# Kernel optimization log

Hardware: AMD Instinct MI355X
Metric: run time of the kernel (lower is better)

## Reference

```python
import jax, jax.numpy as jnp
import numpy as np

N, E, P, D, G, L = 100000, 640000, 640000, 128, 128, 3
BN_EPS = 1e-5

def _bn(x, p):
    # eval-mode BatchNorm1d: p is stacked [gamma, beta, running_mean, running_var]
    g, b, m, v = p[0], p[1], p[2], p[3]
    return (x - m) * jax.lax.rsqrt(v + BN_EPS) * g + b

def setup_inputs() -> dict:
    key = jax.random.key(0)
    ks = iter(jax.random.split(key, 64))
    def nrm(shape, s):
        return jax.random.normal(next(ks), shape, jnp.float32) * s
    def bnp(shape):
        return jax.random.uniform(next(ks), shape, jnp.float32, 0.5, 1.5)
    inp = {}
    # graph data
    inp['x_node'] = jnp.zeros((N,), jnp.int32)
    inp['edge_index'] = jax.random.randint(next(ks), (2, E), 0, N, jnp.int32)
    inp['edge_attr'] = jax.random.normal(next(ks), (E, 7), jnp.float32)
    inp['batch'] = jnp.sort(jax.random.randint(next(ks), (N,), 0, G, jnp.int32))
    inp['pos_index'] = jax.random.randint(next(ks), (P,), 0, 1800, jnp.int32)
    inp['pos_enc'] = jax.random.uniform(next(ks), (P,), jnp.float32)
    inp['pos_batch'] = jnp.sort(jax.random.randint(next(ks), (P,), 0, E, jnp.int32))
    # encoders
    inp['node_emb'] = nrm((1, D), 1.0)                 # Embedding(1, D) for ogbg-ppa
    inp['z_init'] = nrm((1800, D), 1.0)                # z_initial embedding table
    inp['ze_bn1'] = bnp((4, D))
    inp['ze_W'] = nrm((D, D), D ** -0.5)
    inp['ze_b'] = jnp.zeros((D,), jnp.float32)
    inp['ze_bn2'] = bnp((4, D))
    inp['vn_emb'] = jnp.zeros((1, D), jnp.float32)     # init.constant_(0)
    # GINConv_eff per-layer params (stacked over L)
    inp['conv_We'] = nrm((L, 7, D), 7 ** -0.5)         # edge_encoder Linear(7, D)
    inp['conv_be'] = jnp.zeros((L, D), jnp.float32)
    inp['conv_Wp'] = nrm((L, D, D), D ** -0.5)         # edge_encoder_pos Linear(D, D)
    inp['conv_bp'] = jnp.zeros((L, D), jnp.float32)
    inp['conv_W1'] = nrm((L, D, 2 * D), D ** -0.5)     # mlp Linear(D, 2D)
    inp['conv_b1'] = jnp.zeros((L, 2 * D), jnp.float32)
    inp['conv_bn'] = bnp((L, 4, 2 * D))                # mlp BatchNorm(2D)
    inp['conv_W2'] = nrm((L, 2 * D, D), (2 * D) ** -0.5)  # mlp Linear(2D, D)
    inp['conv_b2'] = jnp.zeros((L, D), jnp.float32)
    inp['conv_eps'] = jnp.zeros((L,), jnp.float32)     # GIN eps, init 0
    inp['layer_bn'] = bnp((L, 4, D))                   # per-layer batch_norms
    # virtual-node MLPs (L-1 of them)
    inp['vn_W1'] = nrm((L - 1, D, 2 * D), D ** -0.5)
    inp['vn_b1'] = jnp.zeros((L - 1, 2 * D), jnp.float32)
    inp['vn_bn1'] = bnp((L - 1, 4, 2 * D))
    inp['vn_W2'] = nrm((L - 1, 2 * D, D), (2 * D) ** -0.5)
    inp['vn_b2'] = jnp.zeros((L - 1, D), jnp.float32)
    inp['vn_bn2'] = bnp((L - 1, 4, D))
    return inp

def reference(x_node, edge_index, edge_attr, batch, pos_index, pos_enc, pos_batch,
              node_emb, z_init, ze_bn1, ze_W, ze_b, ze_bn2, vn_emb,
              conv_We, conv_be, conv_Wp, conv_bp, conv_W1, conv_b1, conv_bn,
              conv_W2, conv_b2, conv_eps, layer_bn,
              vn_W1, vn_b1, vn_bn1, vn_W2, vn_b2, vn_bn2):
    src, dst = edge_index[0], edge_index[1]
    # node encoder (Embedding(1, D) indexed by zeros)
    h = node_emb[x_node]                                           # [N, D]
    # positional edge embedding: pool z_initial rows per edge, then z_embedding MLP
    z = jax.ops.segment_sum(z_init[pos_index] * pos_enc[:, None], pos_batch,
                            num_segments=E)                        # [E, D]
    z = jax.nn.relu(_bn(z, ze_bn1))
    z = jax.nn.relu(_bn(z @ ze_W + ze_b, ze_bn2))
    # virtual node embeddings, one per graph
    vn = jnp.broadcast_to(vn_emb[0], (G, D))
    for l in range(L):
        h_in = h + vn[batch]                                       # virtual-node broadcast add
        # GINConv_eff
        edge_emb = edge_attr @ conv_We[l] + conv_be[l] + z @ conv_Wp[l] + conv_bp[l]  # [E, D]
        msg = jax.nn.relu(h_in[src] + edge_emb)                    # gather + relu
        agg = jax.ops.segment_sum(msg, dst, num_segments=N)        # scatter-add
        t = (1.0 + conv_eps[l]) * h_in + agg
        t = jax.nn.relu(_bn(t @ conv_W1[l] + conv_b1[l], conv_bn[l]))
        out = t @ conv_W2[l] + conv_b2[l]
        out = _bn(out, layer_bn[l])                                # batch_norms[l]
        h = out if l == L - 1 else jax.nn.relu(out)                # dropout is identity (eval)
        if l < L - 1:
            vt = jax.ops.segment_sum(h_in, batch, num_segments=G) + vn
            vt = jax.nn.relu(_bn(vt @ vn_W1[l] + vn_b1[l], vn_bn1[l]))
            vn = jax.nn.relu(_bn(vt @ vn_W2[l] + vn_b2[l], vn_bn2[l]))
    return h  # JK == 'last'
```

## Files before the change

kernel.cpp:

```cpp
#include <hip/hip_runtime.h>
#include <hip/hip_bf16.h>

typedef __hip_bfloat16 bf16;
typedef __attribute__((ext_vector_type(8))) short short8;
typedef __attribute__((ext_vector_type(4))) float floatx4;

constexpr int Nn = 100000;
constexpr int Ee = 640000;
constexpr int Pp = 640000;
constexpr int Gg = 128;
constexpr int Ll = 3;
#define Dd 128
#define BN_EPS 1e-5f

__device__ __forceinline__ float b2f(bf16 x) { return __bfloat162float(x); }
__device__ __forceinline__ bf16 f2b(float x) { return __float2bfloat16(x); }

union U8 { uint4 u; bf16 h[8]; short8 s; };

__global__ void k_estart(const int* __restrict__ pos_batch, int* __restrict__ estart) {
  int e = blockIdx.x * blockDim.x + threadIdx.x;
  if (e > Ee) return;
  int lo = 0, hi = Pp;
  while (lo < hi) { int mid = (lo + hi) >> 1; if (pos_batch[mid] < e) lo = mid + 1; else hi = mid; }
  estart[e] = lo;
}

__global__ void k_hist(const int* __restrict__ dst, int* __restrict__ cnt) {
  int e = blockIdx.x * blockDim.x + threadIdx.x;
  if (e >= Ee) return;
  atomicAdd(&cnt[dst[e]], 1);
}

__global__ void k_scanA(const int* __restrict__ cnt, int* __restrict__ rs,
                        int* __restrict__ chunkSum) {
  __shared__ int buf[1024];
  int tid = threadIdx.x;
  int i = blockIdx.x * 1024 + tid;
  int v = (i < Nn) ? cnt[i] : 0;
  buf[tid] = v;
  __syncthreads();
  for (int off = 1; off < 1024; off <<= 1) {
    int t = (tid >= off) ? buf[tid - off] : 0;
    __syncthreads();
    buf[tid] += t;
    __syncthreads();
  }
  if (i < Nn) rs[i] = buf[tid] - v;
  if (tid == 1023) chunkSum[blockIdx.x] = buf[1023];
}

__global__ void k_scanC(int* __restrict__ rs, const int* __restrict__ chunkSum) {
  __shared__ int offS;
  if (threadIdx.x == 0) {
    int o = 0;
    for (int j = 0; j < blockIdx.x; ++j) o += chunkSum[j];
    offS = o;
  }
  __syncthreads();
  int i = blockIdx.x * 1024 + threadIdx.x;
  if (i < Nn) rs[i] += offS;
}

__global__ void k_scatter(const int* __restrict__ dst, const int* __restrict__ rs,
                          int* __restrict__ cur, int* __restrict__ perm) {
  int e = blockIdx.x * blockDim.x + threadIdx.x;
  if (e >= Ee) return;
  int d = dst[e];
  int r = atomicAdd(&cur[d], 1);
  perm[rs[d] + r] = e;
}

__global__ void k_permcopy(const int* __restrict__ perm, const int* __restrict__ src,
                           const int* __restrict__ dst, const int* __restrict__ estart,
                           const float* __restrict__ eattr,
                           int* __restrict__ src_p, int* __restrict__ dst_p,
                           int2* __restrict__ rng_p, bf16* __restrict__ ea_p) {
  int i = blockIdx.x * blockDim.x + threadIdx.x;
  if (i >= Ee) return;
  int e = perm[i];
  src_p[i] = src[e];
  dst_p[i] = dst[e];
  rng_p[i] = make_int2(estart[e], estart[e + 1]);
  U8 o;
  #pragma unroll
  for (int j = 0; j < 7; ++j) o.h[j] = f2b(eattr[(size_t)e * 7 + j]);
  o.h[7] = f2b(1.0f);
  ((uint4*)ea_p)[i] = o.u;
}

__global__ void k_prep(const float* __restrict__ zeW, const float* __restrict__ Wp,
                       const float* __restrict__ We, const float* __restrict__ be,
                       const float* __restrict__ bp,
                       const float* __restrict__ W1, const float* __restrict__ W2,
                       bf16* __restrict__ zeWsw, bf16* __restrict__ WpSw,
                       bf16* __restrict__ WeSw, bf16* __restrict__ W1sw,
                       bf16* __restrict__ W2sw) {
  int gid = blockIdx.x * blockDim.x + threadIdx.x;
  if (gid < 16384) {
    int i = gid;
    int j = i & 7, lane = (i >> 3) & 63, t = (i >> 9) & 7, kc = i >> 12;
    int k = kc * 32 + ((lane >> 4) * 8) + j, n = t * 16 + (lane & 15);
    zeWsw[i] = f2b(zeW[k * 128 + n]);
  }
  if (gid < 49152) {
    int l = gid / 16384, i = gid % 16384;
    int j = i & 7, lane = (i >> 3) & 63, t = (i >> 9) & 7, kc = i >> 12;
    int k = kc * 32 + ((lane >> 4) * 8) + j, n = t * 16 + (lane & 15);
    WpSw[gid] = f2b(Wp[l * 16384 + k * 128 + n]);
  }
  if (gid < 12288) {
    int l = gid / 4096, i = gid % 4096;
    int j = i & 7, lane = (i >> 3) & 63, t = i >> 9;
    int k = ((lane >> 4) * 8) + j, n = t * 16 + (lane & 15);
    float v = 0.f;
    if (k < 7) v = We[l * 896 + k * 128 + n];
    else if (k == 7) v = be[l * 128 + n] + bp[l * 128 + n];
    WeSw[gid] = f2b(v);
  }
  if (gid < 98304) {
    int l = gid / 32768, i = gid % 32768;
    int j = i & 7, lane = (i >> 3) & 63, t = (i >> 9) & 15, kc = i >> 13;
    int k = kc * 32 + ((lane >> 4) * 8) + j, n = t * 16 + (lane & 15);
    W1sw[gid] = f2b(W1[l * 32768 + k * 256 + n]);
  }
  if (gid < 98304) {
    int l = gid / 32768, i = gid % 32768;
    int j = i & 7, lane = (i >> 3) & 63, t = (i >> 9) & 7, kc = i >> 12;
    int k = kc * 32 + ((lane >> 4) * 8) + j, n = t * 16 + (lane & 15);
    W2sw[gid] = f2b(W2[l * 32768 + k * 128 + n]);
  }
}

__global__ void k_bnfold(const float* __restrict__ ze_bn1, const float* __restrict__ ze_b,
                         const float* __restrict__ ze_bn2,
                         const float* __restrict__ conv_b1, const float* __restrict__ conv_bn,
                         const float* __restrict__ conv_b2, const float* __restrict__ layer_bn,
                         const float* __restrict__ vn_b1, const float* __restrict__ vn_bn1,
                         const float* __restrict__ vn_b2, const float* __restrict__ vn_bn2,
                         float* __restrict__ fb) {
  int i = blockIdx.x * blockDim.x + threadIdx.x;
  if (i < 128) {
    float g = ze_bn1[i], b = ze_bn1[128 + i], m = ze_bn1[256 + i], v = ze_bn1[384 + i];
    float s = g * rsqrtf(v + BN_EPS);
    fb[i] = s; fb[128 + i] = b - m * s;
  } else if (i < 256) {
    int c = i - 128;
    float g = ze_bn2[c], b = ze_bn2[128 + c], m = ze_bn2[256 + c], v = ze_bn2[384 + c];
    float s = g * rsqrtf(v + BN_EPS);
    fb[256 + c] = s; fb[384 + c] = b - m * s + s * ze_b[c];
  } else if (i < 1024) {
    int j = i - 256; int l = j >> 8, c = j & 255;
    const float* bn = conv_bn + (size_t)l * 1024;
    float g = bn[c], b = bn[256 + c], m = bn[512 + c], v = bn[768 + c];
    float s = g * rsqrtf(v + BN_EPS);
    fb[512 + j] = s; fb[1280 + j] = b - m * s + s * conv_b1[l * 256 + c];
  } else if (i < 1408) {
    int j = i - 1024; int l = j >> 7, c = j & 127;
    const float* bn = layer_bn + (size_t)l * 512;
    float g = bn[c], b = bn[128 + c], m = bn[256 + c], v = bn[384 + c];
    float s = g * rsqrtf(v + BN_EPS);
    fb[2048 + j] = s; fb[2432 + j] = b - m * s + s * conv_b2[l * 128 + c];
  } else if (i < 1920) {
    int j = i - 1408; int l = j >> 8, c = j & 255;
    const float* bn = vn_bn1 + (size_t)l * 1024;
    float g = bn[c], b = bn[256 + c], m = bn[512 + c], v = bn[768 + c];
    float s = g * rsqrtf(v + BN_EPS);
    fb[2816 + j] = s; fb[3328 + j] = b - m * s + s * vn_b1[l * 256 + c];
  } else if (i < 2176) {
    int j = i - 1920; int l = j >> 7, c = j & 127;
    const float* bn = vn_bn2 + (size_t)l * 512;
    float g = bn[c], b = bn[128 + c], m = bn[256 + c], v = bn[384 + c];
    float s = g * rsqrtf(v + BN_EPS);
    fb[3840 + j] = s; fb[4096 + j] = b - m * s + s * vn_b2[l * 128 + c];
  }
}

__global__ void k_init_vn(const float* __restrict__ vn_emb, float* __restrict__ vn) {
  int gid = blockIdx.x * blockDim.x + threadIdx.x;
  if (gid >= Gg * 128) return;
  vn[gid] = vn_emb[gid & 127];
}

__global__ void k_hin0(const int* __restrict__ x_node, const float* __restrict__ node_emb,
                       const float* __restrict__ vn, const int* __restrict__ batch,
                       bf16* __restrict__ h_in) {
  int gid = blockIdx.x * blockDim.x + threadIdx.x;
  if (gid >= Nn * 16) return;
  int n = gid >> 4, c = gid & 15;
  int x = x_node[n], b = batch[n];
  float4 a0 = ((const float4*)node_emb)[x * 32 + c * 2];
  float4 a1 = ((const float4*)node_emb)[x * 32 + c * 2 + 1];
  float4 v0 = ((const float4*)vn)[b * 32 + c * 2];
  float4 v1 = ((const float4*)vn)[b * 32 + c * 2 + 1];
  U8 o;
  o.h[0] = f2b(a0.x + v0.x); o.h[1] = f2b(a0.y + v0.y);
  o.h[2] = f2b(a0.z + v0.z); o.h[3] = f2b(a0.w + v0.w);
  o.h[4] = f2b(a1.x + v1.x); o.h[5] = f2b(a1.y + v1.y);
  o.h[6] = f2b(a1.z + v1.z); o.h[7] = f2b(a1.w + v1.w);
  ((uint4*)h_in)[gid] = o.u;
}

__global__ void k_hin(const float* __restrict__ vn, const int* __restrict__ batch,
                      bf16* __restrict__ h_in) {
  int gid = blockIdx.x * blockDim.x + threadIdx.x;
  if (gid >= Nn * 16) return;
  int n = gid >> 4, c = gid & 15;
  U8 a; a.u = ((const uint4*)h_in)[gid];
  int b = batch[n];
  float4 v0 = ((const float4*)vn)[b * 32 + c * 2];
  float4 v1 = ((const float4*)vn)[b * 32 + c * 2 + 1];
  U8 o;
  o.h[0] = f2b(b2f(a.h[0]) + v0.x); o.h[1] = f2b(b2f(a.h[1]) + v0.y);
  o.h[2] = f2b(b2f(a.h[2]) + v0.z); o.h[3] = f2b(b2f(a.h[3]) + v0.w);
  o.h[4] = f2b(b2f(a.h[4]) + v1.x); o.h[5] = f2b(b2f(a.h[5]) + v1.y);
  o.h[6] = f2b(b2f(a.h[6]) + v1.z); o.h[7] = f2b(b2f(a.h[7]) + v1.w);
  ((uint4*)h_in)[gid] = o.u;
}

__global__ __launch_bounds__(256, 4) void k_zemb(
    const int2* __restrict__ rng_perm, const int* __restrict__ pos_index,
    const float* __restrict__ pos_enc, const float* __restrict__ z_init,
    const float* __restrict__ fb, const bf16* __restrict__ zeWsw,
    bf16* __restrict__ Z) {
  __shared__ bf16 Az[64][136];
  int tid = threadIdx.x;
  int lane = tid & 63, wv = tid >> 6;
  int q = lane >> 4, ln = lane & 15;
  int e0 = blockIdx.x * 64;

  {
    int r = lane >> 2, cc = lane & 3;
    int2 rg = rng_perm[e0 + 16 * wv + r];
    float acc[32];
    #pragma unroll
    for (int j = 0; j < 32; ++j) acc[j] = 0.f;
    for (int p = rg.x; p < rg.y; ++p) {
      int idx = pos_index[p];
      float w = pos_enc[p];
      #pragma unroll
      for (int qq = 0; qq < 8; ++qq) {
        float4 z4 = ((const float4*)z_init)[idx * 32 + cc * 8 + qq];
        acc[qq * 4 + 0] = fmaf(w, z4.x, acc[qq * 4 + 0]);
        acc[qq * 4 + 1] = fmaf(w, z4.y, acc[qq * 4 + 1]);
        acc[qq * 4 + 2] = fmaf(w, z4.z, acc[qq * 4 + 2]);
        acc[qq * 4 + 3] = fmaf(w, z4.w, acc[qq * 4 + 3]);
      }
    }
    #pragma unroll
    for (int qq = 0; qq < 4; ++qq) {
      U8 o;
      #pragma unroll
      for (int jj = 0; jj < 2; ++jj) {
        int col = cc * 32 + qq * 8 + jj * 4;
        float4 s4 = *(const float4*)&fb[col];
        float4 h4 = *(const float4*)&fb[128 + col];
        o.h[jj * 4 + 0] = f2b(fmaxf(0.f, fmaf(acc[qq * 8 + jj * 4 + 0], s4.x, h4.x)));
        o.h[jj * 4 + 1] = f2b(fmaxf(0.f, fmaf(acc[qq * 8 + jj * 4 + 1], s4.y, h4.y)));
        o.h[jj * 4 + 2] = f2b(fmaxf(0.f, fmaf(acc[qq * 8 + jj * 4 + 2], s4.z, h4.z)));
        o.h[jj * 4 + 3] = f2b(fmaxf(0.f, fmaf(acc[qq * 8 + jj * 4 + 3], s4.w, h4.w)));
      }
      *(uint4*)&Az[16 * wv + r][cc * 32 + qq * 8] = o.u;
    }
  }
  __builtin_amdgcn_wave_barrier();

  floatx4 acc1[8] = {};
  #pragma unroll
  for (int kc = 0; kc < 4; ++kc) {
    short8 af = *(const short8*)&Az[16 * wv + ln][kc * 32 + q * 8];
    #pragma unroll
    for (int t = 0; t < 8; ++t) {
      short8 bfr = *(const short8*)(zeWsw + (((size_t)kc * 8 + t) * 64 + lane) * 8);
      acc1[t] = __builtin_amdgcn_mfma_f32_16x16x32_bf16(af, bfr, acc1[t], 0, 0, 0);
    }
  }
  #pragma unroll
  for (int t = 0; t < 8; ++t) {
    int c = t * 16 + ln;
    float ss = fb[256 + c], hh = fb[384 + c];
    #pragma unroll
    for (int r = 0; r < 4; ++r)
      Az[16 * wv + q * 4 + r][c] = f2b(fmaxf(0.f, fmaf(acc1[t][r], ss, hh)));
  }
  __builtin_amdgcn_wave_barrier();
  #pragma unroll
  for (int p = 0; p < 4; ++p) {
    int row = 16 * wv + p * 4 + q;
    uint4 vv = *(const uint4*)&Az[row][ln * 8];
    ((uint4*)Z)[(size_t)(e0 + row) * 16 + ln] = vv;
  }
}

__global__ __launch_bounds__(256, 6) void k_edge_fused(
    const bf16* __restrict__ Z, const bf16* __restrict__ ea_p,
    const int* __restrict__ src_p, const int* __restrict__ dst_p,
    const bf16* __restrict__ h_in,
    const bf16* __restrict__ WpSw, const bf16* __restrict__ WeSw,
    float* agg) {
  __shared__ bf16 Az[64][136];
  __shared__ int dstS[64];
  int tid = threadIdx.x;
  int lane = tid & 63, wv = tid >> 6;
  int q = lane >> 4, ln = lane & 15;
  int e0 = blockIdx.x * 64;

  if (q == 0) dstS[16 * wv + ln] = dst_p[e0 + 16 * wv + ln];

  short8 af0 = {};
  if (q == 0) af0 = *(const short8*)(ea_p + (size_t)(e0 + 16 * wv + ln) * 8);
  const bf16* zrow = Z + (size_t)(e0 + 16 * wv + ln) * 128 + q * 8;
  short8 zf0 = *(const short8*)(zrow);
  short8 zf1 = *(const short8*)(zrow + 32);
  short8 zf2 = *(const short8*)(zrow + 64);
  short8 zf3 = *(const short8*)(zrow + 96);

  #pragma unroll
  for (int p = 0; p < 4; ++p) {
    int el = 16 * wv + p * 4 + q;
    int s = src_p[e0 + el];
    uint4 hh = ((const uint4*)h_in)[(size_t)s * 16 + ln];
    *(uint4*)&Az[el][ln * 8] = hh;
  }

  floatx4 acc2[8] = {};
  #pragma unroll
  for (int t = 0; t < 8; ++t) {
    short8 bfr = *(const short8*)(WeSw + ((size_t)t * 64 + lane) * 8);
    acc2[t] = __builtin_amdgcn_mfma_f32_16x16x32_bf16(af0, bfr, acc2[t], 0, 0, 0);
  }
  #pragma unroll
  for (int t = 0; t < 8; ++t) {
    short8 bfr = *(const short8*)(WpSw + ((size_t)t * 64 + lane) * 8);
    acc2[t] = __builtin_amdgcn_mfma_f32_16x16x32_bf16(zf0, bfr, acc2[t], 0, 0, 0);
  }
  #pragma unroll
  for (int t = 0; t < 8; ++t) {
    short8 bfr = *(const short8*)(WpSw + (((size_t)8 + t) * 64 + lane) * 8);
    acc2[t] = __builtin_amdgcn_mfma_f32_16x16x32_bf16(zf1, bfr, acc2[t], 0, 0, 0);
  }
  #pragma unroll
  for (int t = 0; t < 8; ++t) {
    short8 bfr = *(const short8*)(WpSw + (((size_t)16 + t) * 64 + lane) * 8);
    acc2[t] = __builtin_amdgcn_mfma_f32_16x16x32_bf16(zf2, bfr, acc2[t], 0, 0, 0);
  }
  #pragma unroll
  for (int t = 0; t < 8; ++t) {
    short8 bfr = *(const short8*)(WpSw + (((size_t)24 + t) * 64 + lane) * 8);
    acc2[t] = __builtin_amdgcn_mfma_f32_16x16x32_bf16(zf3, bfr, acc2[t], 0, 0, 0);
  }
  __builtin_amdgcn_wave_barrier();
  #pragma unroll
  for (int t = 0; t < 8; ++t) {
    int c = t * 16 + ln;
    #pragma unroll
    for (int r = 0; r < 4; ++r) {
      int el = 16 * wv + q * 4 + r;
      Az[el][c] = f2b(fmaxf(0.f, acc2[t][r] + b2f(Az[el][c])));
    }
  }
  __builtin_amdgcn_wave_barrier();
  {
    float s0 = 0.f, s1 = 0.f;
    int dprev = dstS[16 * wv];
    bool inside = false;
    #pragma unroll
    for (int j = 0; j < 16; ++j) {
      int dcur = dstS[16 * wv + j];
      if (dcur != dprev) {
        float* ap = agg + (size_t)dprev * Dd;
        if (inside) { ap[lane] = s0; ap[64 + lane] = s1; }
        else        { atomicAdd(ap + lane, s0); atomicAdd(ap + 64 + lane, s1); }
        s0 = 0.f; s1 = 0.f; dprev = dcur; inside = true;
      }
      s0 += b2f(Az[16 * wv + j][lane]);
      s1 += b2f(Az[16 * wv + j][64 + lane]);
    }
    float* ap = agg + (size_t)dprev * Dd;
    atomicAdd(ap + lane, s0);
    atomicAdd(ap + 64 + lane, s1);
  }
}

__global__ __launch_bounds__(256, 4) void k_edge_full(
    const int2* __restrict__ rng_perm, const int* __restrict__ pos_index,
    const float* __restrict__ pos_enc, const float* __restrict__ z_init,
    const float* __restrict__ fb, const bf16* __restrict__ zeWsw,
    const bf16* __restrict__ ea_p, const int* __restrict__ src_p,
    const int* __restrict__ dst_p, const bf16* __restrict__ h_in,
    const bf16* __restrict__ WpSw, const bf16* __restrict__ WeSw,
    float* agg) {
  __shared__ bf16 Az[64][136];
  __shared__ int dstS[64];
  int tid = threadIdx.x;
  int lane = tid & 63, wv = tid >> 6;
  int q = lane >> 4, ln = lane & 15;
  int e0 = blockIdx.x * 64;

  if (q == 0) dstS[16 * wv + ln] = dst_p[e0 + 16 * wv + ln];
  short8 af0 = {};
  if (q == 0) af0 = *(const short8*)(ea_p + (size_t)(e0 + 16 * wv + ln) * 8);

  {
    int r = lane >> 2, cc = lane & 3;
    int2 rg = rng_perm[e0 + 16 * wv + r];
    float acc[32];
    #pragma unroll
    for (int j = 0; j < 32; ++j) acc[j] = 0.f;
    for (int p = rg.x; p < rg.y; ++p) {
      int idx = pos_index[p];
      float w = pos_enc[p];
      #pragma unroll
      for (int qq = 0; qq < 8; ++qq) {
        float4 z4 = ((const float4*)z_init)[idx * 32 + cc * 8 + qq];
        acc[qq * 4 + 0] = fmaf(w, z4.x, acc[qq * 4 + 0]);
        acc[qq * 4 + 1] = fmaf(w, z4.y, acc[qq * 4 + 1]);
        acc[qq * 4 + 2] = fmaf(w, z4.z, acc[qq * 4 + 2]);
        acc[qq * 4 + 3] = fmaf(w, z4.w, acc[qq * 4 + 3]);
      }
    }
    #pragma unroll
    for (int qq = 0; qq < 4; ++qq) {
      U8 o;
      #pragma unroll
      for (int jj = 0; jj < 2; ++jj) {
        int col = cc * 32 + qq * 8 + jj * 4;
        float4 s4 = *(const float4*)&fb[col];
        float4 h4 = *(const float4*)&fb[128 + col];
        o.h[jj * 4 + 0] = f2b(fmaxf(0.f, fmaf(acc[qq * 8 + jj * 4 + 0], s4.x, h4.x)));
        o.h[jj * 4 + 1] = f2b(fmaxf(0.f, fmaf(acc[qq * 8 + jj * 4 + 1], s4.y, h4.y)));
        o.h[jj * 4 + 2] = f2b(fmaxf(0.f, fmaf(acc[qq * 8 + jj * 4 + 2], s4.z, h4.z)));
        o.h[jj * 4 + 3] = f2b(fmaxf(0.f, fmaf(acc[qq * 8 + jj * 4 + 3], s4.w, h4.w)));
      }
      *(uint4*)&Az[16 * wv + r][cc * 32 + qq * 8] = o.u;
    }
  }
  __builtin_amdgcn_wave_barrier();

  floatx4 acc2[8] = {};
  #pragma unroll
  for (int t = 0; t < 8; ++t) {
    short8 bfr = *(const short8*)(WeSw + ((size_t)t * 64 + lane) * 8);
    acc2[t] = __builtin_amdgcn_mfma_f32_16x16x32_bf16(af0, bfr, acc2[t], 0, 0, 0);
  }
  floatx4 acc1[8] = {};
  #pragma unroll
  for (int kc = 0; kc < 4; ++kc) {
    short8 af = *(const short8*)&Az[16 * wv + ln][kc * 32 + q * 8];
    #pragma unroll
    for (int t = 0; t < 8; ++t) {
      short8 bfr = *(const short8*)(zeWsw + (((size_t)kc * 8 + t) * 64 + lane) * 8);
      acc1[t] = __builtin_amdgcn_mfma_f32_16x16x32_bf16(af, bfr, acc1[t], 0, 0, 0);
    }
  }
  #pragma unroll
  for (int t = 0; t < 8; ++t) {
    int c = t * 16 + ln;
    float ss = fb[256 + c], hh = fb[384 + c];
    #pragma unroll
    for (int r = 0; r < 4; ++r)
      Az[16 * wv + q * 4 + r][c] = f2b(fmaxf(0.f, fmaf(acc1[t][r], ss, hh)));
  }
  __builtin_amdgcn_wave_barrier();
  #pragma unroll
  for (int kc = 0; kc < 4; ++kc) {
    short8 af = *(const short8*)&Az[16 * wv + ln][kc * 32 + q * 8];
    #pragma unroll
    for (int t = 0; t < 8; ++t) {
      short8 bfr = *(const short8*)(WpSw + (((size_t)kc * 8 + t) * 64 + lane) * 8);
      acc2[t] = __builtin_amdgcn_mfma_f32_16x16x32_bf16(af, bfr, acc2[t], 0, 0, 0);
    }
  }
  __builtin_amdgcn_wave_barrier();
  #pragma unroll
  for (int p = 0; p < 4; ++p) {
    int el = 16 * wv + p * 4 + q;
    int s = src_p[e0 + el];
    uint4 hh = ((const uint4*)h_in)[(size_t)s * 16 + ln];
    *(uint4*)&Az[el][ln * 8] = hh;
  }
  __builtin_amdgcn_wave_barrier();
  #pragma unroll
  for (int t = 0; t < 8; ++t) {
    int c = t * 16 + ln;
    #pragma unroll
    for (int r = 0; r < 4; ++r) {
      int el = 16 * wv + q * 4 + r;
      Az[el][c] = f2b(fmaxf(0.f, acc2[t][r] + b2f(Az[el][c])));
    }
  }
  __builtin_amdgcn_wave_barrier();
  {
    float s0 = 0.f, s1 = 0.f;
    int dprev = dstS[16 * wv];
    bool inside = false;
    #pragma unroll
    for (int j = 0; j < 16; ++j) {
      int dcur = dstS[16 * wv + j];
      if (dcur != dprev) {
        float* ap = agg + (size_t)dprev * Dd;
        if (inside) { ap[lane] = s0; ap[64 + lane] = s1; }
        else        { atomicAdd(ap + lane, s0); atomicAdd(ap + 64 + lane, s1); }
        s0 = 0.f; s1 = 0.f; dprev = dcur; inside = true;
      }
      s0 += b2f(Az[16 * wv + j][lane]);
      s1 += b2f(Az[16 * wv + j][64 + lane]);
    }
    float* ap = agg + (size_t)dprev * Dd;
    atomicAdd(ap + lane, s0);
    atomicAdd(ap + 64 + lane, s1);
  }
}

__global__ __launch_bounds__(256) void k_mlp_fused(
    const bf16* __restrict__ h_in, const float* agg,
    const float* __restrict__ eps_arr, int l,
    const bf16* __restrict__ W1sw, const float* __restrict__ Msc, const float* __restrict__ Msh,
    const bf16* __restrict__ W2sw, const float* __restrict__ Lsc, const float* __restrict__ Lsh,
    int is_last, bf16* __restrict__ out_b, float* out_f) {
  __shared__ bf16 R[4][16][280];
  int tid = threadIdx.x;
  int lane = tid & 63, wv = tid >> 6;
  int q = lane >> 4, ln = lane & 15;
  int r0 = blockIdx.x * 64;
  float epsv = 1.0f + eps_arr[l];
  {
    int r = lane >> 2, cc = lane & 3;
    int row = r0 + 16 * wv + r;
    #pragma unroll
    for (int u = 0; u < 4; ++u) {
      int cb = cc * 4 + u;
      U8 o;
      if (row < Nn) {
        U8 hh; hh.u = ((const uint4*)h_in)[row * 16 + cb];
        float4 g0 = ((const float4*)agg)[row * 32 + cb * 2];
        float4 g1 = ((const float4*)agg)[row * 32 + cb * 2 + 1];
        o.h[0] = f2b(epsv * b2f(hh.h[0]) + g0.x); o.h[1] = f2b(epsv * b2f(hh.h[1]) + g0.y);
        o.h[2] = f2b(epsv * b2f(hh.h[2]) + g0.z); o.h[3] = f2b(epsv * b2f(hh.h[3]) + g0.w);
        o.h[4] = f2b(epsv * b2f(hh.h[4]) + g1.x); o.h[5] = f2b(epsv * b2f(hh.h[5]) + g1.y);
        o.h[6] = f2b(epsv * b2f(hh.h[6]) + g1.z); o.h[7] = f2b(epsv * b2f(hh.h[7]) + g1.w);
      } else {
        o.u.x = o.u.y = o.u.z = o.u.w = 0;
      }
      *(uint4*)&R[wv][r][cb * 8] = o.u;
    }
  }
  __builtin_amdgcn_wave_barrier();
  floatx4 acc1[16] = {};
  #pragma unroll
  for (int kc = 0; kc < 4; ++kc) {
    short8 af = *(const short8*)&R[wv][ln][kc * 32 + q * 8];
    #pragma unroll
    for (int t = 0; t < 16; ++t) {
      short8 bfr = *(const short8*)(W1sw + (size_t)l * 32768 + (((size_t)kc * 16 + t) * 64 + lane) * 8);
      acc1[t] = __builtin_amdgcn_mfma_f32_16x16x32_bf16(af, bfr, acc1[t], 0, 0, 0);
    }
  }
  #pragma unroll
  for (int t = 0; t < 16; ++t) {
    int c = t * 16 + ln;
    float ss = Msc[c], hh = Msh[c];
    #pragma unroll
    for (int r = 0; r < 4; ++r)
      R[wv][q * 4 + r][c] = f2b(fmaxf(0.f, fmaf(acc1[t][r], ss, hh)));
  }
  __builtin_amdgcn_wave_barrier();
  floatx4 acc2[8] = {};
  #pragma unroll
  for (int kc = 0; kc < 8; ++kc) {
    short8 af = *(const short8*)&R[wv][ln][kc * 32 + q * 8];
    #pragma unroll
    for (int t = 0; t < 8; ++t) {
      short8 bfr = *(const short8*)(W2sw + (size_t)l * 32768 + (((size_t)kc * 8 + t) * 64 + lane) * 8);
      acc2[t] = __builtin_amdgcn_mfma_f32_16x16x32_bf16(af, bfr, acc2[t], 0, 0, 0);
    }
  }
  #pragma unroll
  for (int t = 0; t < 8; ++t) {
    int c = t * 16 + ln;
    float ss = Lsc[c], hh = Lsh[c];
    #pragma unroll
    for (int r = 0; r < 4; ++r) {
      int row = r0 + 16 * wv + q * 4 + r;
      if (row < Nn) {
        float x = fmaf(acc2[t][r], ss, hh);
        if (is_last) out_f[(size_t)row * Dd + c] = x;
        else         out_b[(size_t)row * Dd + c] = f2b(fmaxf(0.f, x));
      }
    }
  }
}

__global__ void k_vt_sum(const bf16* __restrict__ h_in, const int* __restrict__ batch,
                         float* __restrict__ vt) {
  int d = threadIdx.x;
  int chunk = (Nn + gridDim.x - 1) / gridDim.x;
  int r0 = blockIdx.x * chunk;
  int r1 = min(r0 + chunk, Nn);
  if (r0 >= r1) return;
  float acc = 0.f;
  int cur = batch[r0];
  for (int r = r0; r < r1; ++r) {
    int g = batch[r];
    if (g != cur) { atomicAdd(&vt[cur * Dd + d], acc); acc = 0.f; cur = g; }
    acc += b2f(h_in[r * Dd + d]);
  }
  atomicAdd(&vt[cur * Dd + d], acc);
}

__global__ __launch_bounds__(256) void k_vn_mlp(
    float* __restrict__ vn, const float* __restrict__ vt,
    const float* __restrict__ W1, const float* __restrict__ s1, const float* __restrict__ h1,
    const float* __restrict__ W2, const float* __restrict__ s2, const float* __restrict__ h2) {
  __shared__ float row[128];
  __shared__ float trow[256];
  int g = blockIdx.x;
  int tid = threadIdx.x;
  if (tid < 128) row[tid] = vt[g * Dd + tid] + vn[g * Dd + tid];
  __syncthreads();
  float acc = 0.f;
  for (int k = 0; k < 128; ++k) acc += row[k] * W1[k * 256 + tid];
  trow[tid] = fmaxf(0.f, fmaf(acc, s1[tid], h1[tid]));
  __syncthreads();
  if (tid < 128) {
    float acc2 = 0.f;
    for (int k = 0; k < 256; ++k) acc2 += trow[k] * W2[k * Dd + tid];
    vn[g * Dd + tid] = fmaxf(0.f, fmaf(acc2, s2[tid], h2[tid]));
  }
}

extern "C" void kernel_launch(void* const* d_in, const int* in_sizes, int n_in,
                              void* d_out, int out_size, void* d_ws, size_t ws_size,
                              hipStream_t stream) {
  const int*   x_node    = (const int*)  d_in[0];
  const int*   edge_idx  = (const int*)  d_in[1];
  const float* edge_attr = (const float*)d_in[2];
  const int*   batch     = (const int*)  d_in[3];
  const int*   pos_index = (const int*)  d_in[4];
  const float* pos_enc   = (const float*)d_in[5];
  const int*   pos_batch = (const int*)  d_in[6];
  const float* node_emb  = (const float*)d_in[7];
  const float* z_init    = (const float*)d_in[8];
  const float* ze_bn1    = (const float*)d_in[9];
  const float* ze_W      = (const float*)d_in[10];
  const float* ze_b      = (const float*)d_in[11];
  const float* ze_bn2    = (const float*)d_in[12];
  const float* vn_emb    = (const float*)d_in[13];
  const float* conv_We   = (const float*)d_in[14];
  const float* conv_be   = (const float*)d_in[15];
  const float* conv_Wp   = (const float*)d_in[16];
  const float* conv_bp   = (const float*)d_in[17];
  const float* conv_W1   = (const float*)d_in[18];
  const float* conv_b1   = (const float*)d_in[19];
  const float* conv_bn   = (const float*)d_in[20];
  const float* conv_W2   = (const float*)d_in[21];
  const float* conv_b2   = (const float*)d_in[22];
  const float* conv_eps  = (const float*)d_in[23];
  const float* layer_bn  = (const float*)d_in[24];
  const float* vn_W1     = (const float*)d_in[25];
  const float* vn_b1     = (const float*)d_in[26];
  const float* vn_bn1    = (const float*)d_in[27];
  const float* vn_W2     = (const float*)d_in[28];
  const float* vn_b2     = (const float*)d_in[29];
  const float* vn_bn2    = (const float*)d_in[30];

  char* wb = (char*)d_ws;
  size_t o = 0;
  auto alloc = [&](size_t bytes) { void* p = wb + o; o += (bytes + 255) & ~255ull; return p; };
  bf16*  h_in     = (bf16*) alloc((size_t)Nn * 128 * 2);
  float* vn       = (float*)alloc((size_t)Gg * 128 * 4);
  float* vt       = (float*)alloc((size_t)Gg * 128 * 4);
  int*   estart   = (int*)  alloc((size_t)(Ee + 1) * 4);
  bf16*  zeWsw    = (bf16*) alloc(16384 * 2);
  bf16*  WpSw     = (bf16*) alloc(49152 * 2);
  bf16*  WeSw     = (bf16*) alloc(12288 * 2);
  bf16*  W1sw     = (bf16*) alloc(98304 * 2);
  bf16*  W2sw     = (bf16*) alloc(98304 * 2);
  float* fb       = (float*)alloc(4352 * 4);
  int*   cnt      = (int*)  alloc((size_t)Nn * 4);
  int*   rs       = (int*)  alloc((size_t)Nn * 4);
  int*   cur      = (int*)  alloc((size_t)Nn * 4);
  int*   chunkSum = (int*)  alloc(128 * 4);
  int*   perm     = (int*)  alloc((size_t)Ee * 4);
  int*   src_p    = (int*)  alloc((size_t)Ee * 4);
  int*   dst_p    = (int*)  alloc((size_t)Ee * 4);
  int2*  rng_p    = (int2*) alloc((size_t)Ee * 8);
  bf16*  ea_p     = (bf16*) alloc((size_t)Ee * 8 * 2);
  bf16*  Z        = (bf16*) alloc((size_t)Ee * 128 * 2);
  float* agg      = (float*)d_out;
  bool useZ = (o <= ws_size);

  const int* src = edge_idx;
  const int* dst = edge_idx + Ee;

  k_estart<<<(Ee + 256) / 256, 256, 0, stream>>>(pos_batch, estart);
  hipMemsetAsync(cnt, 0, (size_t)Nn * 4, stream);
  hipMemsetAsync(cur, 0, (size_t)Nn * 4, stream);
  k_hist<<<(Ee + 255) / 256, 256, 0, stream>>>(dst, cnt);
  int nchunk = (Nn + 1023) / 1024;
  k_scanA<<<nchunk, 1024, 0, stream>>>(cnt, rs, chunkSum);
  k_scanC<<<nchunk, 1024, 0, stream>>>(rs, chunkSum);
  k_scatter<<<(Ee + 255) / 256, 256, 0, stream>>>(dst, rs, cur, perm);
  k_permcopy<<<(Ee + 255) / 256, 256, 0, stream>>>(perm, src, dst, estart, edge_attr,
                                                   src_p, dst_p, rng_p, ea_p);
  k_prep<<<(98304 + 255) / 256, 256, 0, stream>>>(ze_W, conv_Wp, conv_We, conv_be, conv_bp,
                                                  conv_W1, conv_W2,
                                                  zeWsw, WpSw, WeSw, W1sw, W2sw);
  k_bnfold<<<9, 256, 0, stream>>>(ze_bn1, ze_b, ze_bn2, conv_b1, conv_bn,
                                  conv_b2, layer_bn, vn_b1, vn_bn1, vn_b2, vn_bn2, fb);
  k_init_vn<<<(Gg * 128 + 255) / 256, 256, 0, stream>>>(vn_emb, vn);
  if (useZ)
    k_zemb<<<Ee / 64, 256, 0, stream>>>(rng_p, pos_index, pos_enc, z_init, fb, zeWsw, Z);

  int hblocks = (Nn * 16 + 255) / 256;
  int mblocks = (Nn + 63) / 64;
  for (int l = 0; l < Ll; ++l) {
    if (l == 0) k_hin0<<<hblocks, 256, 0, stream>>>(x_node, node_emb, vn, batch, h_in);
    else        k_hin <<<hblocks, 256, 0, stream>>>(vn, batch, h_in);
    hipMemsetAsync(agg, 0, (size_t)Nn * 128 * 4, stream);
    if (useZ)
      k_edge_fused<<<Ee / 64, 256, 0, stream>>>(Z, ea_p, src_p, dst_p, h_in,
          WpSw + (size_t)l * 16384, WeSw + (size_t)l * 4096, agg);
    else
      k_edge_full<<<Ee / 64, 256, 0, stream>>>(rng_p, pos_index, pos_enc, z_init,
          fb, zeWsw, ea_p, src_p, dst_p, h_in,
          WpSw + (size_t)l * 16384, WeSw + (size_t)l * 4096, agg);
    if (l < Ll - 1) {
      hipMemsetAsync(vt, 0, (size_t)Gg * 128 * 4, stream);
      k_vt_sum<<<1024, 128, 0, stream>>>(h_in, batch, vt);
      k_vn_mlp<<<Gg, 256, 0, stream>>>(vn, vt,
          vn_W1 + (size_t)l * 128 * 256, fb + 2816 + l * 256, fb + 3328 + l * 256,
          vn_W2 + (size_t)l * 256 * 128, fb + 3840 + l * 128, fb + 4096 + l * 128);
    }
    k_mlp_fused<<<mblocks, 256, 0, stream>>>(h_in, agg, conv_eps, l,
        W1sw, fb + 512 + l * 256, fb + 1280 + l * 256,
        W2sw, fb + 2048 + l * 128, fb + 2432 + l * 128,
        (l == Ll - 1) ? 1 : 0, h_in, (float*)d_out);
  }
}
```

Measured before the change: 1.257 ms.

## Fuse z-embedding into first edge layer and fold vn-add and agg zeroing into MLP

The separate z-embedding kernel is merged into the first layer's edge kernel, which now computes Z, optionally stores it for later layers, and performs the message/aggregation step in the same launch. The per-layer h_in virtual-node add kernel is removed: k_mlp_fused adds vn[batch] to its output and zeroes agg rows as it consumes them, replacing the per-layer memset. This cuts several full passes over node and edge arrays and a few launches. In exchange the MLP epilogue carries extra gathers, and correctness depends on vn being updated before k_mlp_fused runs, which the stream order provides.

```diff
diff --git a/kernel.cpp b/kernel.cpp
--- a/kernel.cpp
+++ b/kernel.cpp
@@ -201,33 +201,24 @@
   ((uint4*)h_in)[gid] = o.u;
 }
 
-__global__ void k_hin(const float* __restrict__ vn, const int* __restrict__ batch,
-                      bf16* __restrict__ h_in) {
-  int gid = blockIdx.x * blockDim.x + threadIdx.x;
-  if (gid >= Nn * 16) return;
-  int n = gid >> 4, c = gid & 15;
-  U8 a; a.u = ((const uint4*)h_in)[gid];
-  int b = batch[n];
-  float4 v0 = ((const float4*)vn)[b * 32 + c * 2];
-  float4 v1 = ((const float4*)vn)[b * 32 + c * 2 + 1];
-  U8 o;
-  o.h[0] = f2b(b2f(a.h[0]) + v0.x); o.h[1] = f2b(b2f(a.h[1]) + v0.y);
-  o.h[2] = f2b(b2f(a.h[2]) + v0.z); o.h[3] = f2b(b2f(a.h[3]) + v0.w);
-  o.h[4] = f2b(b2f(a.h[4]) + v1.x); o.h[5] = f2b(b2f(a.h[5]) + v1.y);
-  o.h[6] = f2b(b2f(a.h[6]) + v1.z); o.h[7] = f2b(b2f(a.h[7]) + v1.w);
-  ((uint4*)h_in)[gid] = o.u;
-}
-
-__global__ __launch_bounds__(256, 4) void k_zemb(
+__global__ __launch_bounds__(256, 4) void k_edge_z(
     const int2* __restrict__ rng_perm, const int* __restrict__ pos_index,
     const float* __restrict__ pos_enc, const float* __restrict__ z_init,
     const float* __restrict__ fb, const bf16* __restrict__ zeWsw,
-    bf16* __restrict__ Z) {
+    const bf16* __restrict__ ea_p, const int* __restrict__ src_p,
+    const int* __restrict__ dst_p, const bf16* __restrict__ h_in,
+    const bf16* __restrict__ WpSw, const bf16* __restrict__ WeSw,
+    bf16* __restrict__ Z, int store_z, float* agg) {
   __shared__ bf16 Az[64][136];
+  __shared__ int dstS[64];
   int tid = threadIdx.x;
   int lane = tid & 63, wv = tid >> 6;
   int q = lane >> 4, ln = lane & 15;
   int e0 = blockIdx.x * 64;
+
+  if (q == 0) dstS[16 * wv + ln] = dst_p[e0 + 16 * wv + ln];
+  short8 af0 = {};
+  if (q == 0) af0 = *(const short8*)(ea_p + (size_t)(e0 + 16 * wv + ln) * 8);
 
   {
     int r = lane >> 2, cc = lane & 3;
@@ -265,6 +256,12 @@
   }
   __builtin_amdgcn_wave_barrier();
 
+  floatx4 acc2[8] = {};
+  #pragma unroll
+  for (int t = 0; t < 8; ++t) {
+    short8 bfr = *(const short8*)(WeSw + ((size_t)t * 64 + lane) * 8);
+    acc2[t] = __builtin_amdgcn_mfma_f32_16x16x32_bf16(af0, bfr, acc2[t], 0, 0, 0);
+  }
   floatx4 acc1[8] = {};
   #pragma unroll
   for (int kc = 0; kc < 4; ++kc) {
@@ -285,10 +282,61 @@
   }
   __builtin_amdgcn_wave_barrier();
   #pragma unroll
+  for (int kc = 0; kc < 4; ++kc) {
+    short8 af = *(const short8*)&Az[16 * wv + ln][kc * 32 + q * 8];
+    #pragma unroll
+    for (int t = 0; t < 8; ++t) {
+      short8 bfr = *(const short8*)(WpSw + (((size_t)kc * 8 + t) * 64 + lane) * 8);
+      acc2[t] = __builtin_amdgcn_mfma_f32_16x16x32_bf16(af, bfr, acc2[t], 0, 0, 0);
+    }
+  }
+  __builtin_amdgcn_wave_barrier();
+  if (store_z) {
+    #pragma unroll
+    for (int p = 0; p < 4; ++p) {
+      int row = 16 * wv + p * 4 + q;
+      uint4 vv = *(const uint4*)&Az[row][ln * 8];
+      ((uint4*)Z)[(size_t)(e0 + row) * 16 + ln] = vv;
+    }
+  }
+  __builtin_amdgcn_wave_barrier();
+  #pragma unroll
   for (int p = 0; p < 4; ++p) {
-    int row = 16 * wv + p * 4 + q;
-    uint4 vv = *(const uint4*)&Az[row][ln * 8];
-    ((uint4*)Z)[(size_t)(e0 + row) * 16 + ln] = vv;
+    int el = 16 * wv + p * 4 + q;
+    int s = src_p[e0 + el];
+    uint4 hh = ((const uint4*)h_in)[(size_t)s * 16 + ln];
+    *(uint4*)&Az[el][ln * 8] = hh;
+  }
+  __builtin_amdgcn_wave_barrier();
+  #pragma unroll
+  for (int t = 0; t < 8; ++t) {
+    int c = t * 16 + ln;
+    #pragma unroll
+    for (int r = 0; r < 4; ++r) {
+      int el = 16 * wv + q * 4 + r;
+      Az[el][c] = f2b(fmaxf(0.f, acc2[t][r] + b2f(Az[el][c])));
+    }
+  }
+  __builtin_amdgcn_wave_barrier();
+  {
+    float s0 = 0.f, s1 = 0.f;
+    int dprev = dstS[16 * wv];
+    bool inside = false;
+    #pragma unroll
+    for (int j = 0; j < 16; ++j) {
+      int dcur = dstS[16 * wv + j];
+      if (dcur != dprev) {
+        float* ap = agg + (size_t)dprev * Dd;
+        if (inside) { ap[lane] = s0; ap[64 + lane] = s1; }
+        else        { atomicAdd(ap + lane, s0); atomicAdd(ap + 64 + lane, s1); }
+        s0 = 0.f; s1 = 0.f; dprev = dcur; inside = true;
+      }
+      s0 += b2f(Az[16 * wv + j][lane]);
+      s1 += b2f(Az[16 * wv + j][64 + lane]);
+    }
+    float* ap = agg + (size_t)dprev * Dd;
+    atomicAdd(ap + lane, s0);
+    atomicAdd(ap + 64 + lane, s1);
   }
 }
 
@@ -382,142 +430,13 @@
   }
 }
 
-__global__ __launch_bounds__(256, 4) void k_edge_full(
-    const int2* __restrict__ rng_perm, const int* __restrict__ pos_index,
-    const float* __restrict__ pos_enc, const float* __restrict__ z_init,
-    const float* __restrict__ fb, const bf16* __restrict__ zeWsw,
-    const bf16* __restrict__ ea_p, const int* __restrict__ src_p,
-    const int* __restrict__ dst_p, const bf16* __restrict__ h_in,
-    const bf16* __restrict__ WpSw, const bf16* __restrict__ WeSw,
-    float* agg) {
-  __shared__ bf16 Az[64][136];
-  __shared__ int dstS[64];
-  int tid = threadIdx.x;
-  int lane = tid & 63, wv = tid >> 6;
-  int q = lane >> 4, ln = lane & 15;
-  int e0 = blockIdx.x * 64;
-
-  if (q == 0) dstS[16 * wv + ln] = dst_p[e0 + 16 * wv + ln];
-  short8 af0 = {};
-  if (q == 0) af0 = *(const short8*)(ea_p + (size_t)(e0 + 16 * wv + ln) * 8);
-
-  {
-    int r = lane >> 2, cc = lane & 3;
-    int2 rg = rng_perm[e0 + 16 * wv + r];
-    float acc[32];
-    #pragma unroll
-    for (int j = 0; j < 32; ++j) acc[j] = 0.f;
-    for (int p = rg.x; p < rg.y; ++p) {
-      int idx = pos_index[p];
-      float w = pos_enc[p];
-      #pragma unroll
-      for (int qq = 0; qq < 8; ++qq) {
-        float4 z4 = ((const float4*)z_init)[idx * 32 + cc * 8 + qq];
-        acc[qq * 4 + 0] = fmaf(w, z4.x, acc[qq * 4 + 0]);
-        acc[qq * 4 + 1] = fmaf(w, z4.y, acc[qq * 4 + 1]);
-        acc[qq * 4 + 2] = fmaf(w, z4.z, acc[qq * 4 + 2]);
-        acc[qq * 4 + 3] = fmaf(w, z4.w, acc[qq * 4 + 3]);
-      }
-    }
-    #pragma unroll
-    for (int qq = 0; qq < 4; ++qq) {
-      U8 o;
-      #pragma unroll
-      for (int jj = 0; jj < 2; ++jj) {
-        int col = cc * 32 + qq * 8 + jj * 4;
-        float4 s4 = *(const float4*)&fb[col];
-        float4 h4 = *(const float4*)&fb[128 + col];
-        o.h[jj * 4 + 0] = f2b(fmaxf(0.f, fmaf(acc[qq * 8 + jj * 4 + 0], s4.x, h4.x)));
-        o.h[jj * 4 + 1] = f2b(fmaxf(0.f, fmaf(acc[qq * 8 + jj * 4 + 1], s4.y, h4.y)));
-        o.h[jj * 4 + 2] = f2b(fmaxf(0.f, fmaf(acc[qq * 8 + jj * 4 + 2], s4.z, h4.z)));
-        o.h[jj * 4 + 3] = f2b(fmaxf(0.f, fmaf(acc[qq * 8 + jj * 4 + 3], s4.w, h4.w)));
-      }
-      *(uint4*)&Az[16 * wv + r][cc * 32 + qq * 8] = o.u;
-    }
-  }
-  __builtin_amdgcn_wave_barrier();
-
-  floatx4 acc2[8] = {};
-  #pragma unroll
-  for (int t = 0; t < 8; ++t) {
-    short8 bfr = *(const short8*)(WeSw + ((size_t)t * 64 + lane) * 8);
-    acc2[t] = __builtin_amdgcn_mfma_f32_16x16x32_bf16(af0, bfr, acc2[t], 0, 0, 0);
-  }
-  floatx4 acc1[8] = {};
-  #pragma unroll
-  for (int kc = 0; kc < 4; ++kc) {
-    short8 af = *(const short8*)&Az[16 * wv + ln][kc * 32 + q * 8];
-    #pragma unroll
-    for (int t = 0; t < 8; ++t) {
-      short8 bfr = *(const short8*)(zeWsw + (((size_t)kc * 8 + t) * 64 + lane) * 8);
-      acc1[t] = __builtin_amdgcn_mfma_f32_16x16x32_bf16(af, bfr, acc1[t], 0, 0, 0);
-    }
-  }
-  #pragma unroll
-  for (int t = 0; t < 8; ++t) {
-    int c = t * 16 + ln;
-    float ss = fb[256 + c], hh = fb[384 + c];
-    #pragma unroll
-    for (int r = 0; r < 4; ++r)
-      Az[16 * wv + q * 4 + r][c] = f2b(fmaxf(0.f, fmaf(acc1[t][r], ss, hh)));
-  }
-  __builtin_amdgcn_wave_barrier();
-  #pragma unroll
-  for (int kc = 0; kc < 4; ++kc) {
-    short8 af = *(const short8*)&Az[16 * wv + ln][kc * 32 + q * 8];
-    #pragma unroll
-    for (int t = 0; t < 8; ++t) {
-      short8 bfr = *(const short8*)(WpSw + (((size_t)kc * 8 + t) * 64 + lane) * 8);
-      acc2[t] = __builtin_amdgcn_mfma_f32_16x16x32_bf16(af, bfr, acc2[t], 0, 0, 0);
-    }
-  }
-  __builtin_amdgcn_wave_barrier();
-  #pragma unroll
-  for (int p = 0; p < 4; ++p) {
-    int el = 16 * wv + p * 4 + q;
-    int s = src_p[e0 + el];
-    uint4 hh = ((const uint4*)h_in)[(size_t)s * 16 + ln];
-    *(uint4*)&Az[el][ln * 8] = hh;
-  }
-  __builtin_amdgcn_wave_barrier();
-  #pragma unroll
-  for (int t = 0; t < 8; ++t) {
-    int c = t * 16 + ln;
-    #pragma unroll
-    for (int r = 0; r < 4; ++r) {
-      int el = 16 * wv + q * 4 + r;
-      Az[el][c] = f2b(fmaxf(0.f, acc2[t][r] + b2f(Az[el][c])));
-    }
-  }
-  __builtin_amdgcn_wave_barrier();
-  {
-    float s0 = 0.f, s1 = 0.f;
-    int dprev = dstS[16 * wv];
-    bool inside = false;
-    #pragma unroll
-    for (int j = 0; j < 16; ++j) {
-      int dcur = dstS[16 * wv + j];
-      if (dcur != dprev) {
-        float* ap = agg + (size_t)dprev * Dd;
-        if (inside) { ap[lane] = s0; ap[64 + lane] = s1; }
-        else        { atomicAdd(ap + lane, s0); atomicAdd(ap + 64 + lane, s1); }
-        s0 = 0.f; s1 = 0.f; dprev = dcur; inside = true;
-      }
-      s0 += b2f(Az[16 * wv + j][lane]);
-      s1 += b2f(Az[16 * wv + j][64 + lane]);
-    }
-    float* ap = agg + (size_t)dprev * Dd;
-    atomicAdd(ap + lane, s0);
-    atomicAdd(ap + 64 + lane, s1);
-  }
-}
-
 __global__ __launch_bounds__(256) void k_mlp_fused(
-    const bf16* __restrict__ h_in, const float* agg,
+    const bf16* __restrict__ h_in, float* agg,
     const float* __restrict__ eps_arr, int l,
+    const int* __restrict__ batch, const float* __restrict__ vn,
     const bf16* __restrict__ W1sw, const float* __restrict__ Msc, const float* __restrict__ Msh,
     const bf16* __restrict__ W2sw, const float* __restrict__ Lsc, const float* __restrict__ Lsh,
-    int is_last, bf16* __restrict__ out_b, float* out_f) {
+    int is_last, int zero_agg, bf16* __restrict__ out_b, float* out_f) {
   __shared__ bf16 R[4][16][280];
   int tid = threadIdx.x;
   int lane = tid & 63, wv = tid >> 6;
@@ -527,6 +446,7 @@
   {
     int r = lane >> 2, cc = lane & 3;
     int row = r0 + 16 * wv + r;
+    float4 z4 = make_float4(0.f, 0.f, 0.f, 0.f);
     #pragma unroll
     for (int u = 0; u < 4; ++u) {
       int cb = cc * 4 + u;
@@ -539,6 +459,10 @@
         o.h[2] = f2b(epsv * b2f(hh.h[2]) + g0.z); o.h[3] = f2b(epsv * b2f(hh.h[3]) + g0.w);
         o.h[4] = f2b(epsv * b2f(hh.h[4]) + g1.x); o.h[5] = f2b(epsv * b2f(hh.h[5]) + g1.y);
         o.h[6] = f2b(epsv * b2f(hh.h[6]) + g1.z); o.h[7] = f2b(epsv * b2f(hh.h[7]) + g1.w);
+        if (zero_agg) {
+          ((float4*)agg)[row * 32 + cb * 2] = z4;
+          ((float4*)agg)[row * 32 + cb * 2 + 1] = z4;
+        }
       } else {
         o.u.x = o.u.y = o.u.z = o.u.w = 0;
       }
@@ -573,6 +497,14 @@
     for (int t = 0; t < 8; ++t) {
       short8 bfr = *(const short8*)(W2sw + (size_t)l * 32768 + (((size_t)kc * 8 + t) * 64 + lane) * 8);
       acc2[t] = __builtin_amdgcn_mfma_f32_16x16x32_bf16(af, bfr, acc2[t], 0, 0, 0);
+    }
+  }
+  int bb[4] = {0, 0, 0, 0};
+  if (!is_last) {
+    #pragma unroll
+    for (int r = 0; r < 4; ++r) {
+      int row = r0 + 16 * wv + q * 4 + r;
+      if (row < Nn) bb[r] = batch[row];
     }
   }
   #pragma unroll
@@ -585,7 +517,7 @@
       if (row < Nn) {
         float x = fmaf(acc2[t][r], ss, hh);
         if (is_last) out_f[(size_t)row * Dd + c] = x;
-        else         out_b[(size_t)row * Dd + c] = f2b(fmaxf(0.f, x));
+        else         out_b[(size_t)row * Dd + c] = f2b(fmaxf(0.f, x) + vn[bb[r] * Dd + c]);
       }
     }
   }
@@ -709,21 +641,18 @@
   k_bnfold<<<9, 256, 0, stream>>>(ze_bn1, ze_b, ze_bn2, conv_b1, conv_bn,
                                   conv_b2, layer_bn, vn_b1, vn_bn1, vn_b2, vn_bn2, fb);
   k_init_vn<<<(Gg * 128 + 255) / 256, 256, 0, stream>>>(vn_emb, vn);
-  if (useZ)
-    k_zemb<<<Ee / 64, 256, 0, stream>>>(rng_p, pos_index, pos_enc, z_init, fb, zeWsw, Z);
-
-  int hblocks = (Nn * 16 + 255) / 256;
+  k_hin0<<<(Nn * 16 + 255) / 256, 256, 0, stream>>>(x_node, node_emb, vn, batch, h_in);
+  hipMemsetAsync(agg, 0, (size_t)Nn * 128 * 4, stream);
+
   int mblocks = (Nn + 63) / 64;
   for (int l = 0; l < Ll; ++l) {
-    if (l == 0) k_hin0<<<hblocks, 256, 0, stream>>>(x_node, node_emb, vn, batch, h_in);
-    else        k_hin <<<hblocks, 256, 0, stream>>>(vn, batch, h_in);
-    hipMemsetAsync(agg, 0, (size_t)Nn * 128 * 4, stream);
-    if (useZ)
+    if (l == 0 || !useZ)
+      k_edge_z<<<Ee / 64, 256, 0, stream>>>(rng_p, pos_index, pos_enc, z_init,
+          fb, zeWsw, ea_p, src_p, dst_p, h_in,
+          WpSw + (size_t)l * 16384, WeSw + (size_t)l * 4096,
+          Z, (l == 0 && useZ) ? 1 : 0, agg);
+    else
       k_edge_fused<<<Ee / 64, 256, 0, stream>>>(Z, ea_p, src_p, dst_p, h_in,
-          WpSw + (size_t)l * 16384, WeSw + (size_t)l * 4096, agg);
-    else
-      k_edge_full<<<Ee / 64, 256, 0, stream>>>(rng_p, pos_index, pos_enc, z_init,
-          fb, zeWsw, ea_p, src_p, dst_p, h_in,
           WpSw + (size_t)l * 16384, WeSw + (size_t)l * 4096, agg);
     if (l < Ll - 1) {
       hipMemsetAsync(vt, 0, (size_t)Gg * 128 * 4, stream);
@@ -732,9 +661,9 @@
           vn_W1 + (size_t)l * 128 * 256, fb + 2816 + l * 256, fb + 3328 + l * 256,
           vn_W2 + (size_t)l * 256 * 128, fb + 3840 + l * 128, fb + 4096 + l * 128);
     }
-    k_mlp_fused<<<mblocks, 256, 0, stream>>>(h_in, agg, conv_eps, l,
+    k_mlp_fused<<<mblocks, 256, 0, stream>>>(h_in, agg, conv_eps, l, batch, vn,
         W1sw, fb + 512 + l * 256, fb + 1280 + l * 256,
         W2sw, fb + 2048 + l * 128, fb + 2432 + l * 128,
-        (l == Ll - 1) ? 1 : 0, h_in, (float*)d_out);
-  }
-}
+        (l == Ll - 1) ? 1 : 0, (l < Ll - 1) ? 1 : 0, h_in, (float*)d_out);
+  }
+}
```

Measured after the change: 1.284 ms. 2.2% more time.
